# Performance work log

Hardware: AMD Instinct MI355X
Metric: run time of the kernel (lower is better)

Reference implementation:

```python
import jax, jax.numpy as jnp
import numpy as np
from jax.scipy.special import xlogy

N = 8192
NUM_CLASSES = 100

def setup_inputs() -> dict:
    key = jax.random.key(0)
    k1, k2, k3 = jax.random.split(key, 3)
    pred1 = jax.random.normal(k1, (N, N), dtype=jnp.float32)
    pred2 = jax.random.normal(k2, (N, N), dtype=jnp.float32)
    labels = jax.random.randint(k3, (N,), 0, NUM_CLASSES, dtype=jnp.int64)
    return {"pred1": pred1, "pred2": pred2, "labels": labels}

def _kl_div_mean(log_input, target):
    # torch.nn.KLDivLoss(reduction='mean'): mean over ALL elements of
    # target * (log(target) - log_input), with 0*log(0) := 0 (xlogy).
    return jnp.mean(xlogy(target, target) - target * log_input)

def reference(pred1, pred2, labels):
    n = pred1.shape[0]
    # vectorized replacement of the python double loop: gt[i,k] = (labels[k]==labels[i])
    gt = (labels[None, :] == labels[:, None]).astype(pred1.dtype)
    probs3 = jax.nn.softmax(gt * 10.0, axis=1)  # [N,N] soft target rows
    logp1 = jax.nn.log_softmax(pred1, axis=1)
    logp2 = jax.nn.log_softmax(pred2, axis=1)
    loss1 = _kl_div_mean(logp1, probs3) * n
    loss2 = _kl_div_mean(logp2, probs3.T) * n
    return (loss1 + loss2) / 2.0
```

## Files before the change

### kernel.cpp

```cpp
#include <hip/hip_runtime.h>
#include <math.h>


constexpr int N_ = 8192;
constexpr int NCLS = 100;
constexpr int NCLSP = 128;
constexpr float E10F = 22026.465794806718f;

__global__ void prep_kernel(const int* __restrict__ labels,
                            int* __restrict__ counts,
                            float* __restrict__ wcls,
                            float* __restrict__ Wout,
                            unsigned char* __restrict__ labu8) {
    __shared__ int cnt[NCLSP];
    int tid = threadIdx.x;
    if (tid < NCLSP) cnt[tid] = 0;
    __syncthreads();
    for (int i = tid; i < N_; i += blockDim.x) {
        int l = labels[i];
        labu8[i] = (unsigned char)l;
        atomicAdd(&cnt[l], 1);
    }
    __syncthreads();
    if (tid < NCLSP) {
        int c = cnt[tid];
        counts[tid] = c;
        float D = (float)c * E10F + (float)(N_ - c);
        wcls[tid] = 1.0f / D;
    }
    if (tid == 0) {
        __syncthreads();
    }
    __syncthreads();
    if (tid == 0) {
        double W = 0.0;
        const double e10 = 22026.465794806718;
        for (int c = 0; c < NCLS; ++c) {
            double cc = (double)cnt[c];
            double D = cc * e10 + ((double)N_ - cc);
            W += cc / D;
        }
        Wout[0] = (float)W;
    }
}

__launch_bounds__(256)
__global__ void row_kernel(const float* __restrict__ pred1,
                           const float* __restrict__ pred2,
                           const int* __restrict__ labels,
                           const uchar4* __restrict__ lab4,
                           const int* __restrict__ counts,
                           const float* __restrict__ wcls,
                           const float* __restrict__ Wptr,
                           float* __restrict__ contrib) {
    const int r = blockIdx.x;
    const int tid = threadIdx.x;
    __shared__ float wsh[NCLSP];
    if (tid < NCLSP) wsh[tid] = wcls[tid];
    const float4* row1 = reinterpret_cast<const float4*>(pred1 + (size_t)r * N_);
    const float4* row2 = reinterpret_cast<const float4*>(pred2 + (size_t)r * N_);
    const int rowlab = labels[r];
    __syncthreads();

    float s1 = 0.f, s2 = 0.f, sum1 = 0.f, sum2 = 0.f, ms1 = 0.f, ms2 = 0.f;
#pragma unroll
    for (int it = 0; it < 8; ++it) {
        const int idx = it * 256 + tid;
        float4 v = row1[idx];
        float4 u = row2[idx];
        uchar4 lb = lab4[idx];

        s1 += __expf(v.x) + __expf(v.y) + __expf(v.z) + __expf(v.w);
        s2 += __expf(u.x) + __expf(u.y) + __expf(u.z) + __expf(u.w);
        sum1 += (v.x + v.y) + (v.z + v.w);

        float w0 = wsh[lb.x], w1 = wsh[lb.y], w2 = wsh[lb.z], w3 = wsh[lb.w];
        sum2 = fmaf(u.x, w0, fmaf(u.y, w1, fmaf(u.z, w2, fmaf(u.w, w3, sum2))));

        bool e0 = ((int)lb.x == rowlab), e1 = ((int)lb.y == rowlab);
        bool e2 = ((int)lb.z == rowlab), e3 = ((int)lb.w == rowlab);
        ms1 += (e0 ? v.x : 0.f) + (e1 ? v.y : 0.f) + (e2 ? v.z : 0.f) + (e3 ? v.w : 0.f);
        ms2 += (e0 ? u.x : 0.f) + (e1 ? u.y : 0.f) + (e2 ? u.z : 0.f) + (e3 ? u.w : 0.f);
    }

#pragma unroll
    for (int mask = 32; mask >= 1; mask >>= 1) {
        s1 += __shfl_xor(s1, mask, 64);
        s2 += __shfl_xor(s2, mask, 64);
        sum1 += __shfl_xor(sum1, mask, 64);
        sum2 += __shfl_xor(sum2, mask, 64);
        ms1 += __shfl_xor(ms1, mask, 64);
        ms2 += __shfl_xor(ms2, mask, 64);
    }

    __shared__ float red[4][6];
    const int wave = tid >> 6;
    if ((tid & 63) == 0) {
        red[wave][0] = s1; red[wave][1] = s2; red[wave][2] = sum1;
        red[wave][3] = sum2; red[wave][4] = ms1; red[wave][5] = ms2;
    }
    __syncthreads();
    if (tid == 0) {
        float S1 = 0.f, S2 = 0.f, SU1 = 0.f, SU2 = 0.f, MS1 = 0.f, MS2 = 0.f;
#pragma unroll
        for (int wv = 0; wv < 4; ++wv) {
            S1 += red[wv][0]; S2 += red[wv][1]; SU1 += red[wv][2];
            SU2 += red[wv][3]; MS1 += red[wv][4]; MS2 += red[wv][5];
        }
        float lse1 = logf(S1);
        float lse2 = logf(S2);
        int cnt = counts[rowlab];
        float w = wcls[rowlab];
        float W = Wptr[0];
        contrib[r] = w * (SU1 - (float)N_ * lse1) +
                     (E10F - 1.0f) * w * (MS1 - (float)cnt * lse1);
        contrib[N_ + r] = (SU2 - lse2 * W) +
                          (E10F - 1.0f) * w * (MS2 - (float)cnt * lse2);
    }
}

__global__ void final_kernel(const int* __restrict__ counts,
                             const float* __restrict__ contrib,
                             float* __restrict__ out) {
    __shared__ double red[256];
    int tid = threadIdx.x;
    double acc = 0.0;
    for (int i = tid; i < 2 * N_; i += 256)
        acc += (double)contrib[i];
    red[tid] = acc;
    __syncthreads();
    for (int st = 128; st > 0; st >>= 1) {
        if (tid < st) red[tid] += red[tid + st];
        __syncthreads();
    }
    if (tid == 0) {
        const double e10 = 22026.465794806718;
        double H = 0.0;
        for (int c = 0; c < NCLS; ++c) {
            double cc = (double)counts[c];
            double D = cc * e10 + ((double)N_ - cc);
            double logD = log(D);
            H += cc * (cc * (e10 / D) * (10.0 - logD) +
                       ((double)N_ - cc) * (1.0 / D) * (-logD));
        }
        out[0] = (float)((2.0 * H - red[0]) / (2.0 * (double)N_));
    }
}

extern "C" void kernel_launch(void* const* d_in, const int* in_sizes, int n_in,
                              void* d_out, int out_size, void* d_ws, size_t ws_size,
                              hipStream_t stream) {
    const float* pred1 = (const float*)d_in[0];
    const float* pred2 = (const float*)d_in[1];
    const int* labels = (const int*)d_in[2];
    float* out = (float*)d_out;

    float* wsf = (float*)d_ws;
    int* wsi = (int*)d_ws;
    int* counts = wsi;
    float* wcls = wsf + 128;
    float* Wptr = wsf + 256;
    unsigned char* labu8 = (unsigned char*)(wsf + 384);
    float* contrib = wsf + 2560;

    prep_kernel<<<1, 1024, 0, stream>>>(labels, counts, wcls, Wptr, labu8);
    row_kernel<<<N_, 256, 0, stream>>>(pred1, pred2, labels,
                                       (const uchar4*)labu8, counts, wcls,
                                       Wptr, contrib);
    final_kernel<<<1, 256, 0, stream>>>(counts, contrib, out);
}
```

Measured before the change: 150.7 us.

## Make row kernel persistent with double-buffered async global-to-LDS tile staging

Result: slower. 161.2 us (+6.9%).

```diff
diff --git a/kernel.cpp b/kernel.cpp
--- a/kernel.cpp
+++ b/kernel.cpp
@@ -6,6 +6,10 @@
 constexpr int NCLS = 100;
 constexpr int NCLSP = 128;
 constexpr float E10F = 22026.465794806718f;
+constexpr int GRID = 2048;
+constexpr int ROWSPB = N_ / GRID;
+constexpr int TILE = 4096;
+constexpr int NSTEP = ROWSPB * 2;
 
 __global__ void prep_kernel(const int* __restrict__ labels,
                             int* __restrict__ counts,
@@ -28,9 +32,6 @@
         float D = (float)c * E10F + (float)(N_ - c);
         wcls[tid] = 1.0f / D;
     }
-    if (tid == 0) {
-        __syncthreads();
-    }
     __syncthreads();
     if (tid == 0) {
         double W = 0.0;
@@ -44,78 +45,124 @@
     }
 }
 
+__device__ __forceinline__ void stage16k(const float* __restrict__ g,
+                                         float* lds, int lane, int wv) {
+#pragma unroll
+    for (int c = 0; c < 4; ++c) {
+        const int chunk = wv + c * 4;
+        __builtin_amdgcn_global_load_lds(
+            (const __attribute__((address_space(1))) void*)(g + chunk * 256 + lane * 4),
+            (__attribute__((address_space(3))) void*)(lds + chunk * 256),
+            16, 0, 0);
+    }
+}
+
 __launch_bounds__(256)
 __global__ void row_kernel(const float* __restrict__ pred1,
                            const float* __restrict__ pred2,
-                           const int* __restrict__ labels,
-                           const uchar4* __restrict__ lab4,
+                           const unsigned char* __restrict__ labu8,
                            const int* __restrict__ counts,
                            const float* __restrict__ wcls,
                            const float* __restrict__ Wptr,
                            float* __restrict__ contrib) {
-    const int r = blockIdx.x;
+    __shared__ float tA[2][TILE];
+    __shared__ float tB[2][TILE];
+    __shared__ unsigned char labs[N_];
+    __shared__ float wshm[NCLSP];
+    __shared__ int cnts[NCLSP];
+    __shared__ float red[4][6];
+
     const int tid = threadIdx.x;
-    __shared__ float wsh[NCLSP];
-    if (tid < NCLSP) wsh[tid] = wcls[tid];
-    const float4* row1 = reinterpret_cast<const float4*>(pred1 + (size_t)r * N_);
-    const float4* row2 = reinterpret_cast<const float4*>(pred2 + (size_t)r * N_);
-    const int rowlab = labels[r];
-    __syncthreads();
-
-    float s1 = 0.f, s2 = 0.f, sum1 = 0.f, sum2 = 0.f, ms1 = 0.f, ms2 = 0.f;
-#pragma unroll
-    for (int it = 0; it < 8; ++it) {
-        const int idx = it * 256 + tid;
-        float4 v = row1[idx];
-        float4 u = row2[idx];
-        uchar4 lb = lab4[idx];
-
-        s1 += __expf(v.x) + __expf(v.y) + __expf(v.z) + __expf(v.w);
-        s2 += __expf(u.x) + __expf(u.y) + __expf(u.z) + __expf(u.w);
-        sum1 += (v.x + v.y) + (v.z + v.w);
-
-        float w0 = wsh[lb.x], w1 = wsh[lb.y], w2 = wsh[lb.z], w3 = wsh[lb.w];
-        sum2 = fmaf(u.x, w0, fmaf(u.y, w1, fmaf(u.z, w2, fmaf(u.w, w3, sum2))));
-
-        bool e0 = ((int)lb.x == rowlab), e1 = ((int)lb.y == rowlab);
-        bool e2 = ((int)lb.z == rowlab), e3 = ((int)lb.w == rowlab);
-        ms1 += (e0 ? v.x : 0.f) + (e1 ? v.y : 0.f) + (e2 ? v.z : 0.f) + (e3 ? v.w : 0.f);
-        ms2 += (e0 ? u.x : 0.f) + (e1 ? u.y : 0.f) + (e2 ? u.z : 0.f) + (e3 ? u.w : 0.f);
-    }
-
-#pragma unroll
-    for (int mask = 32; mask >= 1; mask >>= 1) {
-        s1 += __shfl_xor(s1, mask, 64);
-        s2 += __shfl_xor(s2, mask, 64);
-        sum1 += __shfl_xor(sum1, mask, 64);
-        sum2 += __shfl_xor(sum2, mask, 64);
-        ms1 += __shfl_xor(ms1, mask, 64);
-        ms2 += __shfl_xor(ms2, mask, 64);
-    }
-
-    __shared__ float red[4][6];
-    const int wave = tid >> 6;
-    if ((tid & 63) == 0) {
-        red[wave][0] = s1; red[wave][1] = s2; red[wave][2] = sum1;
-        red[wave][3] = sum2; red[wave][4] = ms1; red[wave][5] = ms2;
-    }
-    __syncthreads();
-    if (tid == 0) {
-        float S1 = 0.f, S2 = 0.f, SU1 = 0.f, SU2 = 0.f, MS1 = 0.f, MS2 = 0.f;
-#pragma unroll
-        for (int wv = 0; wv < 4; ++wv) {
-            S1 += red[wv][0]; S2 += red[wv][1]; SU1 += red[wv][2];
-            SU2 += red[wv][3]; MS1 += red[wv][4]; MS2 += red[wv][5];
-        }
-        float lse1 = logf(S1);
-        float lse2 = logf(S2);
-        int cnt = counts[rowlab];
-        float w = wcls[rowlab];
-        float W = Wptr[0];
-        contrib[r] = w * (SU1 - (float)N_ * lse1) +
-                     (E10F - 1.0f) * w * (MS1 - (float)cnt * lse1);
-        contrib[N_ + r] = (SU2 - lse2 * W) +
-                          (E10F - 1.0f) * w * (MS2 - (float)cnt * lse2);
+    const int lane = tid & 63, wv = tid >> 6;
+    const int bid = blockIdx.x;
+
+#pragma unroll
+    for (int c = wv; c < 8; c += 4)
+        __builtin_amdgcn_global_load_lds(
+            (const __attribute__((address_space(1))) void*)(labu8 + c * 1024 + lane * 16),
+            (__attribute__((address_space(3))) void*)(labs + c * 1024),
+            16, 0, 0);
+    if (tid < NCLSP) {
+        wshm[tid] = wcls[tid];
+        cnts[tid] = counts[tid];
+    }
+    stage16k(pred1 + (size_t)bid * N_, tA[0], lane, wv);
+    stage16k(pred2 + (size_t)bid * N_, tB[0], lane, wv);
+    const float W = Wptr[0];
+    __syncthreads();
+
+    float s1 = 0.f, s2 = 0.f, su1 = 0.f, su2 = 0.f, ms1 = 0.f, ms2 = 0.f;
+
+    for (int s = 0; s < NSTEP; ++s) {
+        const int p = s >> 1, t = s & 1, b = s & 1;
+        const int r = bid + p * GRID;
+
+        if (s + 1 < NSTEP) {
+            const int p2 = (s + 1) >> 1, t2 = (s + 1) & 1;
+            const size_t off = (size_t)(bid + p2 * GRID) * N_ + (size_t)t2 * TILE;
+            stage16k(pred1 + off, tA[(s + 1) & 1], lane, wv);
+            stage16k(pred2 + off, tB[(s + 1) & 1], lane, wv);
+        }
+
+        const int rowlab = (int)labs[r];
+        const int base4 = (t * TILE) >> 2;
+        const float4* A4 = (const float4*)tA[b];
+        const float4* B4 = (const float4*)tB[b];
+        const uchar4* L4 = (const uchar4*)labs;
+
+#pragma unroll
+        for (int k = 0; k < 4; ++k) {
+            const int j = k * 256 + tid;
+            float4 v = A4[j];
+            float4 u = B4[j];
+            uchar4 lb = L4[base4 + j];
+
+            s1 += __expf(v.x) + __expf(v.y) + __expf(v.z) + __expf(v.w);
+            s2 += __expf(u.x) + __expf(u.y) + __expf(u.z) + __expf(u.w);
+            su1 += (v.x + v.y) + (v.z + v.w);
+
+            float w0 = wshm[lb.x], w1 = wshm[lb.y], w2 = wshm[lb.z], w3 = wshm[lb.w];
+            su2 = fmaf(u.x, w0, fmaf(u.y, w1, fmaf(u.z, w2, fmaf(u.w, w3, su2))));
+
+            bool e0 = ((int)lb.x == rowlab), e1 = ((int)lb.y == rowlab);
+            bool e2 = ((int)lb.z == rowlab), e3 = ((int)lb.w == rowlab);
+            ms1 += (e0 ? v.x : 0.f) + (e1 ? v.y : 0.f) + (e2 ? v.z : 0.f) + (e3 ? v.w : 0.f);
+            ms2 += (e0 ? u.x : 0.f) + (e1 ? u.y : 0.f) + (e2 ? u.z : 0.f) + (e3 ? u.w : 0.f);
+        }
+
+        if (t == 1) {
+#pragma unroll
+            for (int mask = 32; mask >= 1; mask >>= 1) {
+                s1 += __shfl_xor(s1, mask, 64);
+                s2 += __shfl_xor(s2, mask, 64);
+                su1 += __shfl_xor(su1, mask, 64);
+                su2 += __shfl_xor(su2, mask, 64);
+                ms1 += __shfl_xor(ms1, mask, 64);
+                ms2 += __shfl_xor(ms2, mask, 64);
+            }
+            if (lane == 0) {
+                red[wv][0] = s1; red[wv][1] = s2; red[wv][2] = su1;
+                red[wv][3] = su2; red[wv][4] = ms1; red[wv][5] = ms2;
+            }
+            __syncthreads();
+            if (tid == 0) {
+                float S1 = 0.f, S2 = 0.f, SU1 = 0.f, SU2 = 0.f, MS1 = 0.f, MS2 = 0.f;
+#pragma unroll
+                for (int q = 0; q < 4; ++q) {
+                    S1 += red[q][0]; S2 += red[q][1]; SU1 += red[q][2];
+                    SU2 += red[q][3]; MS1 += red[q][4]; MS2 += red[q][5];
+                }
+                float lse1 = logf(S1), lse2 = logf(S2);
+                int cnt = cnts[rowlab];
+                float w = wshm[rowlab];
+                contrib[r] = w * (SU1 - (float)N_ * lse1) +
+                             (E10F - 1.0f) * w * (MS1 - (float)cnt * lse1);
+                contrib[N_ + r] = (SU2 - lse2 * W) +
+                                  (E10F - 1.0f) * w * (MS2 - (float)cnt * lse2);
+            }
+            s1 = s2 = su1 = su2 = ms1 = ms2 = 0.f;
+        }
+        __syncthreads();
     }
 }
 
@@ -164,8 +211,7 @@
     float* contrib = wsf + 2560;
 
     prep_kernel<<<1, 1024, 0, stream>>>(labels, counts, wcls, Wptr, labu8);
-    row_kernel<<<N_, 256, 0, stream>>>(pred1, pred2, labels,
-                                       (const uchar4*)labu8, counts, wcls,
-                                       Wptr, contrib);
+    row_kernel<<<GRID, 256, 0, stream>>>(pred1, pred2, labu8, counts, wcls,
+                                         Wptr, contrib);
     final_kernel<<<1, 256, 0, stream>>>(counts, contrib, out);
 }
```
